# Optimization experiments

Hardware: AMD Instinct MI355X
Metric: run time of the kernel (lower is better)

The kernel has to match this reference:

```python
import jax, jax.numpy as jnp
import numpy as np
import math

IMG = 256      # image H = W (img_shape)
N_ANG = 360    # projection views over [0, pi)
N_DET = 256    # radial detector bins
N_SAMP = 256   # samples along each ray
VOX = 2.0      # voxel size / detector bin width in mm (isotropic)
FWHM = 4.0     # gaussian_PSF FWHM in mm


def _gauss_kernel(sigma):
    radius = max(1, int(math.ceil(3.0 * sigma)))
    t = np.arange(-radius, radius + 1, dtype=np.float64)
    k = np.exp(-0.5 * (t / sigma) ** 2)
    return (k / k.sum()).astype(np.float32), radius


def _blur_axis(x, sigma, axis):
    """1-D Gaussian blur with reflect padding along `axis` (static small kernel)."""
    k, r = _gauss_kernel(sigma)
    x = jnp.moveaxis(x, axis, -1)
    L = x.shape[-1]
    pad = [(0, 0)] * (x.ndim - 1) + [(r, r)]
    xp = jnp.pad(x, pad, mode='reflect')
    out = sum(float(k[i]) * xp[..., i:i + L] for i in range(2 * r + 1))
    return jnp.moveaxis(out, -1, axis)


def _blur2d(x, sigma):
    return _blur_axis(_blur_axis(x, sigma, -1), sigma, -2)


def _geometry():
    """Static parallel-beam ray-sampling geometry (bilinear taps, in pixel units)."""
    theta = np.pi * np.arange(N_ANG) / N_ANG
    r = (np.arange(N_DET) - (N_DET - 1) / 2.0) * VOX   # detector offsets [mm]
    s = (np.arange(N_SAMP) - (N_SAMP - 1) / 2.0) * VOX  # depth along ray [mm]
    cos = np.cos(theta)[:, None, None]
    sin = np.sin(theta)[:, None, None]
    x = r[None, :, None] * cos - s[None, None, :] * sin  # (A, D, S) mm
    y = r[None, :, None] * sin + s[None, None, :] * cos
    ix = x / VOX + (IMG - 1) / 2.0
    iy = y / VOX + (IMG - 1) / 2.0
    valid = ((ix >= 0) & (ix <= IMG - 1) & (iy >= 0) & (iy <= IMG - 1)).astype(np.float32)
    j0 = np.clip(np.floor(ix).astype(np.int32), 0, IMG - 2)
    i0 = np.clip(np.floor(iy).astype(np.int32), 0, IMG - 2)
    fx = (ix - j0).astype(np.float32)
    fy = (iy - i0).astype(np.float32)
    return i0, j0, fy, fx, valid

_GEO = tuple(jnp.asarray(a) for a in _geometry())


def _project(img):
    """Parallel-view 2D ray projection: img (B,H,W) -> sinogram (B, N_DET, N_ANG)."""
    i0, j0, fy, fx, valid = _GEO
    v00 = img[:, i0, j0]
    v01 = img[:, i0, j0 + 1]
    v10 = img[:, i0 + 1, j0]
    v11 = img[:, i0 + 1, j0 + 1]
    vals = ((1 - fy) * (1 - fx) * v00 + (1 - fy) * fx * v01
            + fy * (1 - fx) * v10 + fy * fx * v11) * valid
    sino = vals.sum(-1) * VOX          # (B, N_ANG, N_DET), line integral in mm
    return jnp.transpose(sino, (0, 2, 1))  # (B, N_DET, N_ANG)


def setup_inputs() -> dict:
    key = jax.random.key(0)
    k1, k2 = jax.random.split(key)
    image = jax.random.uniform(k1, (2, 1, IMG, IMG), dtype=jnp.float32)
    attenuation_map = jax.random.uniform(k2, (2, 1, IMG, IMG), dtype=jnp.float32)
    return {"image": image, "attenuation_map": attenuation_map}


def reference(image, attenuation_map):
    sqrt_log2 = math.sqrt(math.log(2.0))
    sigma_img = (FWHM / (4.0 * sqrt_log2)) / VOX
    # emission PSF blur (reflect) then project
    img_b = _blur2d(image, sigma_img)
    sino = _project(img_b[:, 0])[:, None]          # (B,1,N_DET,N_ANG)
    # attenuation: wider PSF blur, 0.01 scale, project, exponential scaling
    sigma_att = (FWHM / (2.0 * sqrt_log2)) / VOX
    att_b = _blur2d(attenuation_map, sigma_att) * 0.01
    att_sino = _project(att_b[:, 0])[:, None]
    sino = sino * jnp.exp(-att_sino * VOX)
    # column-wise (detector axis) sinogram PSF
    sino = _blur_axis(sino, sigma_img, -2)
    return sino
```

## Files before the change

### kernel.cpp

```cpp
#include <hip/hip_runtime.h>
#include <math.h>

#define IMG 256
#define N_ANG 360
#define N_DET 256

#define NH_BLOCKS 362
#define NV_BLOCKS (179 * 32)
#define EPS 1e-3f

struct W9 { float w[9]; };
struct AngTab { double c, sn; float cf, snf; float pad0, pad1; };

typedef _Float16 h2 __attribute__((ext_vector_type(2)));

#if __has_builtin(__builtin_amdgcn_fdot2)
__device__ __forceinline__ float fdot2(h2 a, h2 b, float c) {
    return __builtin_amdgcn_fdot2(a, b, c, false);
}
#else
__device__ __forceinline__ float fdot2(h2 a, h2 b, float c) {
    return c + (float)a[0] * (float)b[0] + (float)a[1] * (float)b[1];
}
#endif

__device__ __forceinline__ h2 as_h2(unsigned u) { return __builtin_bit_cast(h2, u); }
__device__ __forceinline__ unsigned pack2(float a, float b) {
    h2 v = { (_Float16)a, (_Float16)b };
    return __builtin_bit_cast(unsigned, v);
}

__device__ __forceinline__ int refl(int i, int L) {
    if (i < 0) i = -i;
    if (i >= L) i = 2 * (L - 1) - i;
    return i;
}

__global__ void tables_k(AngTab* __restrict__ tab) {
    int a = blockIdx.x * blockDim.x + threadIdx.x;
    if (a < N_ANG) {
        double th = M_PI * (double)a / 360.0;
        double c = cos(th), sn = sin(th);
        tab[a].c = c; tab[a].sn = sn;
        tab[a].cf = (float)c; tab[a].snf = (float)sn;
    }
}

__global__ void blur4_k(const float* __restrict__ img, const float* __restrict__ att,
                        float* __restrict__ pk, W9 wi, W9 wa) {
    int x = threadIdx.x, y = blockIdx.x, m = blockIdx.y;
    const float* src = ((m & 1) ? att : img) + (m >> 1) * IMG * IMG;
    const float* w = (m & 1) ? wa.w : wi.w;
    float scale = (m & 1) ? 0.01f : 1.0f;
    float acc = 0.f;
    for (int dy = -4; dy <= 4; ++dy) {
        float wy = w[dy + 4];
        if (wy == 0.f) continue;
        const float* rowp = src + refl(y + dy, IMG) * IMG;
        float ra = 0.f;
        for (int dx = -4; dx <= 4; ++dx) ra += w[dx + 4] * rowp[refl(x + dx, IMG)];
        acc += wy * ra;
    }
    pk[(y * IMG + x) * 4 + m] = acc * scale;
}

__global__ void quad_k(const float4* __restrict__ pk, uint4* __restrict__ quad) {
    int j = threadIdx.x, i = blockIdx.x;
    int jn = min(j + 1, IMG - 1), in_ = min(i + 1, IMG - 1);
    float4 p00 = pk[i * IMG + j],   p01 = pk[i * IMG + jn];
    float4 p10 = pk[in_ * IMG + j], p11 = pk[in_ * IMG + jn];
    uint4 qa, qb;
    qa.x = pack2(p00.x, p01.x); qa.y = pack2(p10.x, p11.x);
    qa.z = pack2(p00.y, p01.y); qa.w = pack2(p10.y, p11.y);
    qb.x = pack2(p00.z, p01.z); qb.y = pack2(p10.z, p11.z);
    qb.z = pack2(p00.w, p01.w); qb.w = pack2(p10.w, p11.w);
    int p = i * IMG + j;
    quad[2 * p] = qa;
    quad[2 * p + 1] = qb;
}

__device__ __forceinline__ void tap_acc(const uint4* __restrict__ quad,
                                        int i0, int j0,
                                        float w00, float w01, float w10, float w11,
                                        float4& acc) {
    h2 wt = { (_Float16)w00, (_Float16)w01 };
    h2 wb = { (_Float16)w10, (_Float16)w11 };
    const uint4* q = quad + 2 * ((i0 << 8) + j0);
    uint4 qa = q[0], qb = q[1];
    acc.x = fdot2(as_h2(qa.x), wt, acc.x);
    acc.x = fdot2(as_h2(qa.y), wb, acc.x);
    acc.y = fdot2(as_h2(qa.z), wt, acc.y);
    acc.y = fdot2(as_h2(qa.w), wb, acc.y);
    acc.z = fdot2(as_h2(qb.x), wt, acc.z);
    acc.z = fdot2(as_h2(qb.y), wb, acc.z);
    acc.w = fdot2(as_h2(qb.z), wt, acc.w);
    acc.w = fdot2(as_h2(qb.w), wb, acc.w);
}

__global__ __launch_bounds__(512) void proj_k(const uint4* __restrict__ quad,
                                              const AngTab* __restrict__ tab,
                                              float4* __restrict__ part4) {
    int t = threadIdx.x;
    int bx = blockIdx.x;

    if (bx < NH_BLOCKS) {
        int d = t & 255, kc = t >> 8;
        int aidx = bx % 181, kt = bx / 181;
        int a = (aidx <= 90) ? aidx : aidx + 179;
        AngTab tb = tab[a];
        float cf = tb.cf, snf = tb.snf;
        float df = (float)d - 127.5f;
        float hx = fmaf(df, cf, 127.5f);
        float hy = fmaf(df, snf, 127.5f);
        int k0 = kt * 128 + kc * 64;

        float4 acc = make_float4(0.f, 0.f, 0.f, 0.f);
        for (int j = 0; j < 64; ++j) {
            int k = k0 + j;
            float kf = (float)k - 127.5f;
            float ixf = fmaf(-kf, snf, hx);
            float iyf = fmaf(kf, cf, hy);
            float vmin = fminf(fminf(ixf, 255.0f - ixf), fminf(iyf, 255.0f - iyf));
            if (!__any(vmin > -EPS)) continue;
            float m = (vmin >= EPS) ? 2.0f : 0.0f;
            if (fabsf(vmin) < EPS) {
                double ss = (double)(2 * k - 255);
                double rr = (double)(2 * d - 255);
                double rc = __dmul_rn(rr, tb.c), rs = __dmul_rn(rr, tb.sn);
                double ixd = __dadd_rn(__dmul_rn(__dsub_rn(rc, __dmul_rn(ss, tb.sn)), 0.5), 127.5);
                double iyd = __dadd_rn(__dmul_rn(__dadd_rn(rs, __dmul_rn(ss, tb.c)), 0.5), 127.5);
                bool v = (ixd >= 0.0) && (ixd <= 255.0) && (iyd >= 0.0) && (iyd <= 255.0);
                m = v ? 2.0f : 0.0f;
            }
            int j0 = (int)ixf; j0 = min(max(j0, 0), 254);
            int i0 = (int)iyf; i0 = min(max(i0, 0), 254);
            float fx = ixf - (float)j0;
            float fy = iyf - (float)i0;
            float gxm = (1.f - fx) * m, fxm = fx * m;
            float gy = 1.f - fy;
            tap_acc(quad, i0, j0, gy * gxm, gy * fxm, fy * gxm, fy * fxm, acc);
        }

        __shared__ float4 red[512];
        red[t] = acc;
        __syncthreads();
        if (t < 256) {
            float4 u = red[t], v = red[t + 256];
            u.x += v.x; u.y += v.y; u.z += v.z; u.w += v.w;
            part4[(kt * N_ANG + a) * N_DET + t] = u;
        }
    } else {
        int idx = bx - NH_BLOCKS;
        int a = 91 + (idx >> 5);
        int dgrp = idx & 31;
        int lane = t & 63, w = t >> 6;
        int d = dgrp * 8 + w;
        AngTab tb = tab[a];
        float cf = tb.cf, snf = tb.snf;
        float df = (float)d - 127.5f;
        float hx = fmaf(df, cf, 127.5f);
        float hy = fmaf(df, snf, 127.5f);

        float4 acc = make_float4(0.f, 0.f, 0.f, 0.f);
        #pragma unroll
        for (int j = 0; j < 4; ++j) {
            int k = j * 64 + lane;
            float kf = (float)k - 127.5f;
            float ixf = fmaf(-kf, snf, hx);
            float iyf = fmaf(kf, cf, hy);
            float vmin = fminf(fminf(ixf, 255.0f - ixf), fminf(iyf, 255.0f - iyf));
            if (!__any(vmin > -EPS)) continue;
            float m = (vmin >= EPS) ? 2.0f : 0.0f;
            if (fabsf(vmin) < EPS) {
                double ss = (double)(2 * k - 255);
                double rr = (double)(2 * d - 255);
                double rc = __dmul_rn(rr, tb.c), rs = __dmul_rn(rr, tb.sn);
                double ixd = __dadd_rn(__dmul_rn(__dsub_rn(rc, __dmul_rn(ss, tb.sn)), 0.5), 127.5);
                double iyd = __dadd_rn(__dmul_rn(__dadd_rn(rs, __dmul_rn(ss, tb.c)), 0.5), 127.5);
                bool v = (ixd >= 0.0) && (ixd <= 255.0) && (iyd >= 0.0) && (iyd <= 255.0);
                m = v ? 2.0f : 0.0f;
            }
            int j0 = (int)ixf; j0 = min(max(j0, 0), 254);
            int i0 = (int)iyf; i0 = min(max(i0, 0), 254);
            float fx = ixf - (float)j0;
            float fy = iyf - (float)i0;
            float gxm = (1.f - fx) * m, fxm = fx * m;
            float gy = 1.f - fy;
            tap_acc(quad, i0, j0, gy * gxm, gy * fxm, fy * gxm, fy * fxm, acc);
        }

        #pragma unroll
        for (int off = 32; off; off >>= 1) {
            acc.x += __shfl_xor(acc.x, off);
            acc.y += __shfl_xor(acc.y, off);
            acc.z += __shfl_xor(acc.z, off);
            acc.w += __shfl_xor(acc.w, off);
        }
        if (lane == 0) {
            int o = a * N_DET + d;
            part4[o] = acc;
            part4[N_ANG * N_DET + o] = make_float4(0.f, 0.f, 0.f, 0.f);
        }
    }
}

__global__ __launch_bounds__(256) void finish_k(const float4* __restrict__ part4,
                                                float* __restrict__ out, W9 wt) {
    int d = threadIdx.x;
    int ba = blockIdx.x;
    int b = ba / N_ANG, a = ba % N_ANG;
    float4 s = make_float4(0.f, 0.f, 0.f, 0.f);
    #pragma unroll
    for (int kt = 0; kt < 2; ++kt) {
        float4 q = part4[(kt * N_ANG + a) * N_DET + d];
        s.x += q.x; s.y += q.y; s.z += q.z; s.w += q.w;
    }
    float si = b ? s.z : s.x;
    float sa = b ? s.w : s.y;
    __shared__ float vb[N_DET];
    vb[d] = si * expf(-sa * 2.0f);
    __syncthreads();
    float acc = 0.f;
    #pragma unroll
    for (int i = -2; i <= 2; ++i) acc += wt.w[i + 2] * vb[refl(d + i, N_DET)];
    out[(b * N_DET + d) * N_ANG + a] = acc;
}

static void gauss_w(W9* wt, double sigma, int r, int pad_to_center4) {
    double tmp[9];
    double s = 0.0;
    for (int i = -r; i <= r; ++i) {
        double v = exp(-0.5 * ((double)i / sigma) * ((double)i / sigma));
        tmp[i + r] = v;
        s += v;
    }
    for (int i = 0; i < 9; ++i) wt->w[i] = 0.f;
    int off = pad_to_center4 ? (4 - r) : 0;
    for (int i = 0; i < 2 * r + 1; ++i) wt->w[i + off] = (float)(tmp[i] / s);
}

extern "C" void kernel_launch(void* const* d_in, const int* in_sizes, int n_in,
                              void* d_out, int out_size, void* d_ws, size_t ws_size,
                              hipStream_t stream) {
    const float* img = (const float*)d_in[0];
    const float* att = (const float*)d_in[1];
    float* out = (float*)d_out;

    char* ws = (char*)d_ws;
    AngTab* tab = (AngTab*)ws;
    float* pk = (float*)(ws + 16384);
    uint4* quad = (uint4*)(ws + 16384 + (1 << 20));
    float4* part4 = (float4*)(ws + 16384 + 3 * (1 << 20));

    double sqrt_log2 = sqrt(log(2.0));
    double sigma_img = 4.0 / (4.0 * sqrt_log2) / 2.0;
    double sigma_att = 4.0 / (2.0 * sqrt_log2) / 2.0;
    W9 wimg_pad, wimg, watt;
    gauss_w(&wimg_pad, sigma_img, 2, 1);
    gauss_w(&wimg, sigma_img, 2, 0);
    gauss_w(&watt, sigma_att, 4, 0);

    tables_k<<<6, 64, 0, stream>>>(tab);
    blur4_k<<<dim3(IMG, 4), IMG, 0, stream>>>(img, att, pk, wimg_pad, watt);
    quad_k<<<IMG, IMG, 0, stream>>>((const float4*)pk, quad);
    proj_k<<<NH_BLOCKS + NV_BLOCKS, 512, 0, stream>>>(quad, tab, part4);
    finish_k<<<2 * N_ANG, N_DET, 0, stream>>>(part4, out, wimg);
}
```

Before: 69.90 us.

## Clip ray sample ranges analytically and fuse finish into horizontal projection blocks

```diff
diff --git a/kernel.cpp b/kernel.cpp
--- a/kernel.cpp
+++ b/kernel.cpp
@@ -5,7 +5,7 @@
 #define N_ANG 360
 #define N_DET 256
 
-#define NH_BLOCKS 362
+#define NH_BLOCKS 181
 #define NV_BLOCKS (179 * 32)
 #define EPS 1e-3f
 
@@ -34,16 +34,6 @@
     if (i < 0) i = -i;
     if (i >= L) i = 2 * (L - 1) - i;
     return i;
-}
-
-__global__ void tables_k(AngTab* __restrict__ tab) {
-    int a = blockIdx.x * blockDim.x + threadIdx.x;
-    if (a < N_ANG) {
-        double th = M_PI * (double)a / 360.0;
-        double c = cos(th), sn = sin(th);
-        tab[a].c = c; tab[a].sn = sn;
-        tab[a].cf = (float)c; tab[a].snf = (float)sn;
-    }
 }
 
 __global__ void blur4_k(const float* __restrict__ img, const float* __restrict__ att,
@@ -64,8 +54,18 @@
     pk[(y * IMG + x) * 4 + m] = acc * scale;
 }
 
-__global__ void quad_k(const float4* __restrict__ pk, uint4* __restrict__ quad) {
+__global__ void quad_k(const float4* __restrict__ pk, uint4* __restrict__ quad,
+                       AngTab* __restrict__ tab) {
     int j = threadIdx.x, i = blockIdx.x;
+    int gid = i * IMG + j;
+    if (gid < N_ANG) {
+        double th = M_PI * (double)gid / 360.0;
+        double c = cos(th), sn = sin(th);
+        AngTab tb;
+        tb.c = c; tb.sn = sn; tb.cf = (float)c; tb.snf = (float)sn;
+        tb.pad0 = 0.f; tb.pad1 = 0.f;
+        tab[gid] = tb;
+    }
     int jn = min(j + 1, IMG - 1), in_ = min(i + 1, IMG - 1);
     float4 p00 = pk[i * IMG + j],   p01 = pk[i * IMG + jn];
     float4 p10 = pk[in_ * IMG + j], p11 = pk[in_ * IMG + jn];
@@ -77,6 +77,23 @@
     int p = i * IMG + j;
     quad[2 * p] = qa;
     quad[2 * p + 1] = qb;
+}
+
+template <typename P>
+__device__ __forceinline__ int lastTrue(P p) {
+    if (!p(0)) return -1;
+    if (p(255)) return 255;
+    int lo = 0, hi = 255;
+    while (lo < hi) { int m = (lo + hi + 1) >> 1; if (p(m)) lo = m; else hi = m - 1; }
+    return lo;
+}
+template <typename P>
+__device__ __forceinline__ int firstTrue(P p) {
+    if (!p(255)) return 256;
+    if (p(0)) return 0;
+    int lo = 0, hi = 255;
+    while (lo < hi) { int m = (lo + hi) >> 1; if (p(m)) hi = m; else lo = m + 1; }
+    return lo;
 }
 
 __device__ __forceinline__ void tap_acc(const uint4* __restrict__ quad,
@@ -99,39 +116,61 @@
 
 __global__ __launch_bounds__(512) void proj_k(const uint4* __restrict__ quad,
                                               const AngTab* __restrict__ tab,
-                                              float4* __restrict__ part4) {
+                                              float4* __restrict__ part4,
+                                              float* __restrict__ out, W9 wblur) {
     int t = threadIdx.x;
     int bx = blockIdx.x;
 
     if (bx < NH_BLOCKS) {
         int d = t & 255, kc = t >> 8;
-        int aidx = bx % 181, kt = bx / 181;
-        int a = (aidx <= 90) ? aidx : aidx + 179;
+        int a = (bx <= 90) ? bx : bx + 179;
         AngTab tb = tab[a];
-        float cf = tb.cf, snf = tb.snf;
-        float df = (float)d - 127.5f;
-        float hx = fmaf(df, cf, 127.5f);
-        float hy = fmaf(df, snf, 127.5f);
-        int k0 = kt * 128 + kc * 64;
+        double rr = (double)(2 * d - 255);
+        double rc = __dmul_rn(rr, tb.c), rs = __dmul_rn(rr, tb.sn);
+
+        auto evIx = [&](int k) -> double {
+            double ss = (double)(2 * k - 255);
+            return __dadd_rn(__dmul_rn(__dsub_rn(rc, __dmul_rn(ss, tb.sn)), 0.5), 127.5);
+        };
+        auto evIy = [&](int k) -> double {
+            double ss = (double)(2 * k - 255);
+            return __dadd_rn(__dmul_rn(__dadd_rn(rs, __dmul_rn(ss, tb.c)), 0.5), 127.5);
+        };
+        int khiA = lastTrue([&](int k) { return evIx(k) >= 0.0; });
+        int kloA = firstTrue([&](int k) { return evIx(k) <= 255.0; });
+        int kloB, khiB;
+        if (tb.c > 0.0) {
+            kloB = firstTrue([&](int k) { return evIy(k) >= 0.0; });
+            khiB = lastTrue([&](int k) { return evIy(k) <= 255.0; });
+        } else {
+            khiB = lastTrue([&](int k) { return evIy(k) >= 0.0; });
+            kloB = firstTrue([&](int k) { return evIy(k) <= 255.0; });
+        }
+        int lo = max(kloA, kloB), hi = min(khiA, khiB);
+        lo = max(lo, kc * 128); hi = min(hi, kc * 128 + 127);
+        if (lo > hi) { lo = 0; hi = -1; }
+
+        int jl = (hi >= lo) ? lo : 0x7fffffff;
+        int jh = (hi >= lo) ? hi : (-0x7fffffff - 1);
+        int en = lo, ex = hi;
+        #pragma unroll
+        for (int off = 32; off; off >>= 1) {
+            jl = min(jl, __shfl_xor(jl, off));
+            jh = max(jh, __shfl_xor(jh, off));
+            en = max(en, __shfl_xor(en, off));
+            ex = min(ex, __shfl_xor(ex, off));
+        }
+
+        float x0f = (float)evIx(128);
+        float y0f = (float)evIy(128);
+        float dxf = -tb.snf, dyf = tb.cf;
 
         float4 acc = make_float4(0.f, 0.f, 0.f, 0.f);
-        for (int j = 0; j < 64; ++j) {
-            int k = k0 + j;
-            float kf = (float)k - 127.5f;
-            float ixf = fmaf(-kf, snf, hx);
-            float iyf = fmaf(kf, cf, hy);
-            float vmin = fminf(fminf(ixf, 255.0f - ixf), fminf(iyf, 255.0f - iyf));
-            if (!__any(vmin > -EPS)) continue;
-            float m = (vmin >= EPS) ? 2.0f : 0.0f;
-            if (fabsf(vmin) < EPS) {
-                double ss = (double)(2 * k - 255);
-                double rr = (double)(2 * d - 255);
-                double rc = __dmul_rn(rr, tb.c), rs = __dmul_rn(rr, tb.sn);
-                double ixd = __dadd_rn(__dmul_rn(__dsub_rn(rc, __dmul_rn(ss, tb.sn)), 0.5), 127.5);
-                double iyd = __dadd_rn(__dmul_rn(__dadd_rn(rs, __dmul_rn(ss, tb.c)), 0.5), 127.5);
-                bool v = (ixd >= 0.0) && (ixd <= 255.0) && (iyd >= 0.0) && (iyd <= 255.0);
-                m = v ? 2.0f : 0.0f;
-            }
+        auto body = [&](int k, bool fast) {
+            float kf = (float)(k - 128);
+            float ixf = fmaf(kf, dxf, x0f);
+            float iyf = fmaf(kf, dyf, y0f);
+            float m = fast ? 2.0f : ((k >= lo && k <= hi) ? 2.0f : 0.0f);
             int j0 = (int)ixf; j0 = min(max(j0, 0), 254);
             int i0 = (int)iyf; i0 = min(max(i0, 0), 254);
             float fx = ixf - (float)j0;
@@ -139,15 +178,39 @@
             float gxm = (1.f - fx) * m, fxm = fx * m;
             float gy = 1.f - fy;
             tap_acc(quad, i0, j0, gy * gxm, gy * fxm, fy * gxm, fy * fxm, acc);
+        };
+        if (jl <= jh) {
+            if (en <= ex) {
+                for (int k = jl; k < en; ++k) body(k, false);
+                for (int k = en; k <= ex; ++k) body(k, true);
+                for (int k = ex + 1; k <= jh; ++k) body(k, false);
+            } else {
+                for (int k = jl; k <= jh; ++k) body(k, false);
+            }
         }
 
         __shared__ float4 red[512];
+        __shared__ float vb[2][N_DET];
         red[t] = acc;
         __syncthreads();
         if (t < 256) {
             float4 u = red[t], v = red[t + 256];
-            u.x += v.x; u.y += v.y; u.z += v.z; u.w += v.w;
-            part4[(kt * N_ANG + a) * N_DET + t] = u;
+            float si0 = u.x + v.x, sa0 = u.y + v.y;
+            float si1 = u.z + v.z, sa1 = u.w + v.w;
+            vb[0][t] = si0 * expf(-sa0 * 2.0f);
+            vb[1][t] = si1 * expf(-sa1 * 2.0f);
+        }
+        __syncthreads();
+        if (t < 256) {
+            float a0 = 0.f, a1 = 0.f;
+            #pragma unroll
+            for (int i = -2; i <= 2; ++i) {
+                int dd = refl(t + i, N_DET);
+                a0 += wblur.w[i + 2] * vb[0][dd];
+                a1 += wblur.w[i + 2] * vb[1][dd];
+            }
+            out[t * N_ANG + a] = a0;
+            out[(N_DET + t) * N_ANG + a] = a1;
         }
     } else {
         int idx = bx - NH_BLOCKS;
@@ -196,25 +259,16 @@
             acc.z += __shfl_xor(acc.z, off);
             acc.w += __shfl_xor(acc.w, off);
         }
-        if (lane == 0) {
-            int o = a * N_DET + d;
-            part4[o] = acc;
-            part4[N_ANG * N_DET + o] = make_float4(0.f, 0.f, 0.f, 0.f);
-        }
+        if (lane == 0) part4[a * N_DET + d] = acc;
     }
 }
 
-__global__ __launch_bounds__(256) void finish_k(const float4* __restrict__ part4,
-                                                float* __restrict__ out, W9 wt) {
+__global__ __launch_bounds__(256) void finish_v_k(const float4* __restrict__ part4,
+                                                  float* __restrict__ out, W9 wt) {
     int d = threadIdx.x;
-    int ba = blockIdx.x;
-    int b = ba / N_ANG, a = ba % N_ANG;
-    float4 s = make_float4(0.f, 0.f, 0.f, 0.f);
-    #pragma unroll
-    for (int kt = 0; kt < 2; ++kt) {
-        float4 q = part4[(kt * N_ANG + a) * N_DET + d];
-        s.x += q.x; s.y += q.y; s.z += q.z; s.w += q.w;
-    }
+    int b = blockIdx.x / 179;
+    int a = 91 + (blockIdx.x % 179);
+    float4 s = part4[a * N_DET + d];
     float si = b ? s.z : s.x;
     float sa = b ? s.w : s.y;
     __shared__ float vb[N_DET];
@@ -260,9 +314,8 @@
     gauss_w(&wimg, sigma_img, 2, 0);
     gauss_w(&watt, sigma_att, 4, 0);
 
-    tables_k<<<6, 64, 0, stream>>>(tab);
     blur4_k<<<dim3(IMG, 4), IMG, 0, stream>>>(img, att, pk, wimg_pad, watt);
-    quad_k<<<IMG, IMG, 0, stream>>>((const float4*)pk, quad);
-    proj_k<<<NH_BLOCKS + NV_BLOCKS, 512, 0, stream>>>(quad, tab, part4);
-    finish_k<<<2 * N_ANG, N_DET, 0, stream>>>(part4, out, wimg);
-}
+    quad_k<<<IMG, IMG, 0, stream>>>((const float4*)pk, quad, tab);
+    proj_k<<<NH_BLOCKS + NV_BLOCKS, 512, 0, stream>>>(quad, tab, part4, out, wimg);
+    finish_v_k<<<2 * 179, N_DET, 0, stream>>>(part4, out, wimg);
+}
```

Result: faster. 67.63 us (-3.2%).
